# Optimization experiments

Measured on AMD Instinct MI355X. Metric: run time of the kernel, lower is better.

Reference implementation:

```python
import jax, jax.numpy as jnp
import numpy as np

B, S, D = 2, 2048, 1024
H = 16
DH = D // H  # 64


def setup_inputs() -> dict:
    key = jax.random.key(0)
    k1, k2, k3, k4, k5 = jax.random.split(key, 5)
    scale = 1.0 / np.sqrt(D)
    return {
        "x": jax.random.normal(k1, (B, S, D), dtype=jnp.float32),
        "w_in": jax.random.normal(k2, (3 * D, D), dtype=jnp.float32) * scale,
        "b_in": jax.random.normal(k3, (3 * D,), dtype=jnp.float32) * 0.02,
        "w_out": jax.random.normal(k4, (D, D), dtype=jnp.float32) * scale,
        "b_out": jax.random.normal(k5, (D,), dtype=jnp.float32) * 0.02,
        "mask": 1,
    }


def reference(x, w_in, b_in, w_out, b_out, mask):
    bs, seq_len, d_emb = x.shape
    # in_proj: torch Linear -> x @ W^T + b
    qkv = jnp.einsum("bsd,ed->bse", x, w_in) + b_in  # (B, S, 3D)
    q, k, v = jnp.split(qkv, 3, axis=-1)
    # (B, S, D) -> (B, H, S, DH)
    def heads(t):
        return t.reshape(bs, seq_len, H, DH).transpose(0, 2, 1, 3)
    q, k, v = heads(q), heads(k), heads(v)
    scores = jnp.einsum("bhqd,bhkd->bhqk", q, k)  # (B, H, S, S)
    if mask:
        causal = jnp.triu(jnp.ones((seq_len, seq_len), dtype=bool), k=1)
        scores = jnp.where(causal, -jnp.inf, scores)
    # original divides after masking; -inf / scale is still -inf
    scores = scores / jnp.sqrt(jnp.asarray(DH, dtype=scores.dtype))
    weights = jax.nn.softmax(scores, axis=-1)
    att = jnp.einsum("bhqk,bhkd->bhqd", weights, v)  # (B, H, S, DH)
    att = att.transpose(0, 2, 1, 3).reshape(bs, seq_len, d_emb)
    out = jnp.einsum("bsd,ed->bse", att, w_out) + b_out
    return out
```

## Files before the change

kernel.cpp:

```cpp
#include <hip/hip_runtime.h>
#include <hip/hip_bf16.h>
#include <stdint.h>


typedef __attribute__((ext_vector_type(8))) short bf16x8;
typedef __attribute__((ext_vector_type(4))) float f32x4;
typedef __attribute__((ext_vector_type(16))) float f32x16;
typedef __attribute__((ext_vector_type(4))) unsigned int u32x4;

typedef const __attribute__((address_space(1))) uint32_t* gp1_t;
typedef __attribute__((address_space(3))) uint32_t* lp3_t;

static __device__ __forceinline__ uint32_t cvtpk(float lo, float hi) {
  uint32_t r;
  asm("v_cvt_pk_bf16_f32 %0, %1, %2" : "=v"(r) : "v"(lo), "v"(hi));
  return r;
}
static __device__ __forceinline__ uint16_t f2b(float x) {
  return (uint16_t)cvtpk(x, x);
}
static __device__ __forceinline__ float fexp2(float x) {
  float r;
  asm("v_exp_f32 %0, %1" : "=v"(r) : "v"(x));
  return r;
}

template <int ISSUES>
static __device__ __forceinline__ void stage64(const uint16_t* __restrict__ g, int gstride,
                                               uint8_t* lds, int t) {
#pragma unroll
  for (int i = 0; i < ISSUES; ++i) {
    int p = i * 256 + t;
    int row = p >> 3, c = p & 7;
    const uint16_t* src = g + row * gstride + ((c ^ (row & 7)) << 3);
    __builtin_amdgcn_global_load_lds((gp1_t)src, (lp3_t)(lds + (p & ~63) * 16), 16, 0, 0);
  }
}

static __device__ __forceinline__ bf16x8 ld_frag(const uint8_t* lds, int row, int chunk) {
  return *(const bf16x8*)(lds + row * 128 + (((chunk) ^ (row & 7)) << 4));
}

__global__ __launch_bounds__(256) void cvt3(const float* __restrict__ a,
                                            const float* __restrict__ b,
                                            const float* __restrict__ c,
                                            uint16_t* __restrict__ oa,
                                            uint16_t* __restrict__ ob,
                                            uint16_t* __restrict__ oc) {
  int i = blockIdx.x * 256 + threadIdx.x;
  const float* src;
  uint16_t* dst;
  int j;
  if (i < 1048576)      { src = a; dst = oa; j = i; }
  else if (i < 1835008) { src = b; dst = ob; j = i - 1048576; }
  else                  { src = c; dst = oc; j = i - 1835008; }
  float4 v = ((const float4*)src)[j];
  uint2 o;
  o.x = cvtpk(v.x, v.y);
  o.y = cvtpk(v.z, v.w);
  ((uint2*)dst)[j] = o;
}

__global__ __launch_bounds__(256) void gemm_qkv(const uint16_t* __restrict__ A,
                                                const uint16_t* __restrict__ W,
                                                const float* __restrict__ bias,
                                                uint16_t* __restrict__ Qb,
                                                uint16_t* __restrict__ Kb,
                                                uint16_t* __restrict__ Vt) {
  __shared__ union {
    uint8_t stage[65536];
    uint16_t ot[128][136];
  } sm;
  int t = threadIdx.x, l = t & 63, w = t >> 6;
  int m0 = blockIdx.y * 128, n0 = blockIdx.x * 128;
  int wr = (w >> 1) * 64, wc = (w & 1) * 64;
  const f32x4 fz = {0.f, 0.f, 0.f, 0.f};
  f32x4 acc[4][4];
#pragma unroll
  for (int i = 0; i < 4; ++i)
#pragma unroll
    for (int j = 0; j < 4; ++j) acc[i][j] = fz;

  const uint16_t* Ab_ = A + m0 * 1024;
  const uint16_t* Wb_ = W + n0 * 1024;
  stage64<4>(Ab_, 1024, sm.stage, t);
  stage64<4>(Wb_, 1024, sm.stage + 16384, t);

  for (int kt = 0; kt < 16; ++kt) {
    int cur = kt & 1;
    uint8_t* curb = sm.stage + (cur << 15);
    asm volatile("s_waitcnt vmcnt(0)" ::: "memory");
    __syncthreads();
    if (kt + 1 < 16) {
      uint8_t* nb = sm.stage + ((cur ^ 1) << 15);
      stage64<4>(Ab_ + (kt + 1) * 64, 1024, nb, t);
      stage64<4>(Wb_ + (kt + 1) * 64, 1024, nb + 16384, t);
    }
#pragma unroll
    for (int ks = 0; ks < 2; ++ks) {
      bf16x8 a[4], b[4];
#pragma unroll
      for (int i = 0; i < 4; ++i) {
        a[i] = ld_frag(curb, wr + i * 16 + (l & 15), ks * 4 + (l >> 4));
        b[i] = ld_frag(curb + 16384, wc + i * 16 + (l & 15), ks * 4 + (l >> 4));
      }
#pragma unroll
      for (int i = 0; i < 4; ++i)
#pragma unroll
        for (int j = 0; j < 4; ++j)
          acc[i][j] = __builtin_amdgcn_mfma_f32_16x16x32_bf16(a[i], b[j], acc[i][j], 0, 0, 0);
    }
  }

  __syncthreads();
  const float CSQ = 0.18033688011112042f;
  int sec = n0 >> 10;
#pragma unroll
  for (int j = 0; j < 4; ++j) {
    int col = wc + j * 16 + (l & 15);
    float bv = bias[n0 + col];
#pragma unroll
    for (int i = 0; i < 4; ++i) {
      int rb = wr + i * 16 + ((l >> 4) << 2);
#pragma unroll
      for (int r = 0; r < 4; ++r) {
        int row = rb + r;
        float v = acc[i][j][r] + bv;
        if (sec == 0) v *= CSQ;
        if (sec == 2) {
          int rowp = (row & ~12) | ((row & 4) << 1) | ((row & 8) >> 1);
          sm.ot[col][rowp] = f2b(v);
        } else {
          sm.ot[row][col] = f2b(v);
        }
      }
    }
  }
  __syncthreads();

  int bb0 = m0 >> 11, sbase = m0 & 2047;
  int h0 = (n0 & 1023) >> 6;
  if (sec < 2) {
    uint16_t* dst0 = (sec == 0) ? Qb : Kb;
    int s_loc = t & 127, hh = t >> 7;
    const uint16_t* src = &sm.ot[s_loc][hh * 64];
    uint16_t* dst = dst0 + (((size_t)((bb0 * 16 + h0 + hh) * 2048 + sbase + s_loc)) << 6);
#pragma unroll
    for (int c = 0; c < 8; ++c)
      *(u32x4*)(dst + c * 8) = *(const u32x4*)(src + c * 8);
  } else {
    int re = t >> 1, scc = t & 1;
    int hh = re >> 6, dh = re & 63;
    const uint16_t* src = &sm.ot[re][scc * 64];
    uint16_t* dst = Vt + ((size_t)((bb0 * 16 + h0 + hh) * 64 + dh)) * 2048 + sbase + scc * 64;
#pragma unroll
    for (int c = 0; c < 8; ++c)
      *(u32x4*)(dst + c * 8) = *(const u32x4*)(src + c * 8);
  }
}

__global__ __launch_bounds__(256) void gemm_out(const uint16_t* __restrict__ A,
                                                const uint16_t* __restrict__ W,
                                                const float* __restrict__ bias,
                                                float* __restrict__ out) {
  __shared__ uint8_t sm[65536];
  int t = threadIdx.x, l = t & 63, w = t >> 6;
  int m0 = blockIdx.y * 128, n0 = blockIdx.x * 128;
  int wr = (w >> 1) * 64, wc = (w & 1) * 64;
  const f32x4 fz = {0.f, 0.f, 0.f, 0.f};
  f32x4 acc[4][4];
#pragma unroll
  for (int i = 0; i < 4; ++i)
#pragma unroll
    for (int j = 0; j < 4; ++j) acc[i][j] = fz;

  const uint16_t* Ab_ = A + m0 * 1024;
  const uint16_t* Wb_ = W + n0 * 1024;
  stage64<4>(Ab_, 1024, sm, t);
  stage64<4>(Wb_, 1024, sm + 16384, t);

  for (int kt = 0; kt < 16; ++kt) {
    int cur = kt & 1;
    uint8_t* curb = sm + (cur << 15);
    asm volatile("s_waitcnt vmcnt(0)" ::: "memory");
    __syncthreads();
    if (kt + 1 < 16) {
      uint8_t* nb = sm + ((cur ^ 1) << 15);
      stage64<4>(Ab_ + (kt + 1) * 64, 1024, nb, t);
      stage64<4>(Wb_ + (kt + 1) * 64, 1024, nb + 16384, t);
    }
#pragma unroll
    for (int ks = 0; ks < 2; ++ks) {
      bf16x8 a[4], b[4];
#pragma unroll
      for (int i = 0; i < 4; ++i) {
        a[i] = ld_frag(curb, wr + i * 16 + (l & 15), ks * 4 + (l >> 4));
        b[i] = ld_frag(curb + 16384, wc + i * 16 + (l & 15), ks * 4 + (l >> 4));
      }
#pragma unroll
      for (int i = 0; i < 4; ++i)
#pragma unroll
        for (int j = 0; j < 4; ++j)
          acc[i][j] = __builtin_amdgcn_mfma_f32_16x16x32_bf16(a[i], b[j], acc[i][j], 0, 0, 0);
    }
  }
#pragma unroll
  for (int j = 0; j < 4; ++j) {
    int e = n0 + wc + j * 16 + (l & 15);
    float bv = bias[e];
#pragma unroll
    for (int i = 0; i < 4; ++i) {
      int mb = m0 + wr + i * 16 + ((l >> 4) << 2);
#pragma unroll
      for (int r = 0; r < 4; ++r) {
        int m = mb + r;
        out[m * 1024 + e] = acc[i][j][r] + bv;
      }
    }
  }
}

__global__ __launch_bounds__(512) void attn(const uint16_t* __restrict__ Qb,
                                            const uint16_t* __restrict__ Kb,
                                            const uint16_t* __restrict__ Vt,
                                            uint16_t* __restrict__ Ab,
                                            const int* __restrict__ maskp) {
  __shared__ uint8_t smem[32768];
  int t = threadIdx.x, l = t & 63, w = t >> 6;
  int hi = l >> 5, ql = l & 31;
  int did = (int)blockIdx.x;
  int xcd = did & 7, idx = did >> 3;
  int bh = xcd * 4 + (idx >> 3);
  int p = idx & 7;
  int g = w >> 2, wg = w & 3;
  bool causal = (*maskp != 0);
  int st = g ? p : 15 - p;
  int ntg = causal ? 2 * (st + 1) : 32;
  int nth = causal ? 2 * (16 - p) : 32;
  int q0w = st * 128 + wg * 32;
  int q = q0w + ql;
  int bb = bh >> 4, h = bh & 15;

  const uint16_t* KpB = Kb + ((size_t)bh << 17);
  const uint16_t* VpB = Vt + ((size_t)bh << 17);

  bf16x8 qf[4];
  const uint16_t* Qp = Qb + (((size_t)bh * 2048 + q) << 6) + hi * 8;
#pragma unroll
  for (int ks = 0; ks < 4; ++ks) qf[ks] = *(const bf16x8*)(Qp + ks * 16);

  f32x16 acco[2];
#pragma unroll
  for (int r = 0; r < 16; ++r) { acco[0][r] = 0.f; acco[1][r] = 0.f; }
  float lsum = 0.f;

  stage64<1>(KpB, 64, smem, t);
  stage64<1>(VpB, 2048, smem + 8192, t);

  for (int tt = 0; tt < nth; ++tt) {
    int cur = tt & 1;
    asm volatile("s_waitcnt vmcnt(0)" ::: "memory");
    __syncthreads();
    if (tt + 1 < nth) {
      uint8_t* nb = smem + ((cur ^ 1) << 14);
      stage64<1>(KpB + ((size_t)(tt + 1) << 12), 64, nb, t);
      stage64<1>(VpB + (tt + 1) * 64, 2048, nb + 8192, t);
    }
    if (tt >= ntg || (causal && tt * 64 > q0w + 31)) continue;

    const uint8_t* Ks = smem + (cur << 14);
    const uint8_t* Vs = Ks + 8192;
    bf16x8 kf[2][4], vf[2][4];
#pragma unroll
    for (int ks = 0; ks < 4; ++ks) {
      kf[0][ks] = ld_frag(Ks, ql,      ks * 2 + hi);
      kf[1][ks] = ld_frag(Ks, 32 + ql, ks * 2 + hi);
      vf[0][ks] = ld_frag(Vs, ql,      ks * 2 + hi);
      vf[1][ks] = ld_frag(Vs, 32 + ql, ks * 2 + hi);
    }

    f32x16 sc[2];
#pragma unroll
    for (int r = 0; r < 16; ++r) { sc[0][r] = 0.f; sc[1][r] = 0.f; }
    __builtin_amdgcn_s_setprio(1);
#pragma unroll
    for (int ks = 0; ks < 4; ++ks)
      sc[0] = __builtin_amdgcn_mfma_f32_32x32x16_bf16(kf[0][ks], qf[ks], sc[0], 0, 0, 0);
#pragma unroll
    for (int ks = 0; ks < 4; ++ks)
      sc[1] = __builtin_amdgcn_mfma_f32_32x32x16_bf16(kf[1][ks], qf[ks], sc[1], 0, 0, 0);
    __builtin_amdgcn_s_setprio(0);

    bool nomask = (!causal) || (tt * 64 + 63 <= q0w);
    int qrel = q - tt * 64;
    float rs0 = 0.f, rs1 = 0.f, rs2 = 0.f, rs3 = 0.f;

#pragma unroll
    for (int r = 0; r < 16; ++r) {
      float v = sc[0][r];
      if (!nomask) {
        int kv = (r & 3) + 8 * (r >> 2) + 4 * hi;
        v = (kv <= qrel) ? v : -1e30f;
      }
      float e = fexp2(v);
      sc[0][r] = e;
      if (r & 1) rs1 += e; else rs0 += e;
    }

    __builtin_amdgcn_s_setprio(1);
#pragma unroll
    for (int ks = 0; ks < 2; ++ks) {
      int a8 = ks * 8;
      u32x4 wv = {cvtpk(sc[0][a8 + 0], sc[0][a8 + 1]),
                  cvtpk(sc[0][a8 + 2], sc[0][a8 + 3]),
                  cvtpk(sc[0][a8 + 4], sc[0][a8 + 5]),
                  cvtpk(sc[0][a8 + 6], sc[0][a8 + 7])};
      bf16x8 af = __builtin_bit_cast(bf16x8, wv);
      acco[0] = __builtin_amdgcn_mfma_f32_32x32x16_bf16(af, vf[0][ks], acco[0], 0, 0, 0);
      acco[1] = __builtin_amdgcn_mfma_f32_32x32x16_bf16(af, vf[1][ks], acco[1], 0, 0, 0);
    }
    __builtin_amdgcn_s_setprio(0);

#pragma unroll
    for (int r = 0; r < 16; ++r) {
      float v = sc[1][r];
      if (!nomask) {
        int kv = 32 + (r & 3) + 8 * (r >> 2) + 4 * hi;
        v = (kv <= qrel) ? v : -1e30f;
      }
      float e = fexp2(v);
      sc[1][r] = e;
      if (r & 1) rs3 += e; else rs2 += e;
    }

    __builtin_amdgcn_s_setprio(1);
#pragma unroll
    for (int ks = 0; ks < 2; ++ks) {
      int a8 = ks * 8;
      u32x4 wv = {cvtpk(sc[1][a8 + 0], sc[1][a8 + 1]),
                  cvtpk(sc[1][a8 + 2], sc[1][a8 + 3]),
                  cvtpk(sc[1][a8 + 4], sc[1][a8 + 5]),
                  cvtpk(sc[1][a8 + 6], sc[1][a8 + 7])};
      bf16x8 af = __builtin_bit_cast(bf16x8, wv);
      acco[0] = __builtin_amdgcn_mfma_f32_32x32x16_bf16(af, vf[0][ks + 2], acco[0], 0, 0, 0);
      acco[1] = __builtin_amdgcn_mfma_f32_32x32x16_bf16(af, vf[1][ks + 2], acco[1], 0, 0, 0);
    }
    __builtin_amdgcn_s_setprio(0);

    lsum += (rs0 + rs1) + (rs2 + rs3);
  }

  lsum += __shfl_xor(lsum, 32);
#pragma unroll
  for (int r = 0; r < 16; ++r) {
    int crow = (r & 3) + 8 * (r >> 2) + 4 * hi;
    float L = __shfl(lsum, crow);
    float inv = 1.0f / L;
    int qg = q0w + crow;
#pragma unroll
    for (int n = 0; n < 2; ++n)
      Ab[(((size_t)(bb * 2048 + qg)) << 10) + h * 64 + n * 32 + ql] = f2b(acco[n][r] * inv);
  }
}

extern "C" void kernel_launch(void* const* d_in, const int* in_sizes, int n_in,
                              void* d_out, int out_size, void* d_ws, size_t ws_size,
                              hipStream_t stream) {
  const float* x     = (const float*)d_in[0];
  const float* w_in  = (const float*)d_in[1];
  const float* b_in  = (const float*)d_in[2];
  const float* w_out = (const float*)d_in[3];
  const float* b_out = (const float*)d_in[4];
  const int*   mask  = (const int*)d_in[5];
  float* out = (float*)d_out;

  uint8_t* ws = (uint8_t*)d_ws;
  uint16_t* xb  = (uint16_t*)(ws);
  uint16_t* wib = (uint16_t*)(ws + (8u << 20));
  uint16_t* wob = (uint16_t*)(ws + (14u << 20));
  uint16_t* Qb  = (uint16_t*)(ws + (16u << 20));
  uint16_t* Kb  = (uint16_t*)(ws + (24u << 20));
  uint16_t* Vt  = (uint16_t*)(ws + (32u << 20));
  uint16_t* Ab  = (uint16_t*)(ws + (40u << 20));

  cvt3<<<8192, 256, 0, stream>>>(x, w_in, w_out, xb, wib, wob);
  gemm_qkv<<<dim3(24, 32), 256, 0, stream>>>(xb, wib, b_in, Qb, Kb, Vt);
  attn<<<256, 512, 0, stream>>>(Qb, Kb, Vt, Ab, mask);
  gemm_out<<<dim3(8, 32), 256, 0, stream>>>(Ab, wob, b_out, out);
}
```

Baseline: 124.8 us.

## Split attention KV range across two warp groups per query tile with LDS reduction

Before this change, each block paired two query tiles (st and 15-p) across its two 4-warp groups to balance causal work. Now each block owns one 128-row query tile, and the two warp groups split its KV range in half, each running its own double-buffered K/V staging. Partial output accumulators and row sums are merged through shared memory at the end. The grid doubles to 512 blocks to expose more parallelism, at the cost of doubled LDS per block (64KB), an extra reduction pass, and uneven block sizes across the causal triangle.

```diff
diff --git a/kernel.cpp b/kernel.cpp
--- a/kernel.cpp
+++ b/kernel.cpp
@@ -225,24 +225,25 @@
                                             const uint16_t* __restrict__ Vt,
                                             uint16_t* __restrict__ Ab,
                                             const int* __restrict__ maskp) {
-  __shared__ uint8_t smem[32768];
+  __shared__ uint8_t smem[65536];
   int t = threadIdx.x, l = t & 63, w = t >> 6;
   int hi = l >> 5, ql = l & 31;
+  int g = w >> 2, wg = w & 3;
+  int tl = t & 255;
   int did = (int)blockIdx.x;
   int xcd = did & 7, idx = did >> 3;
-  int bh = xcd * 4 + (idx >> 3);
-  int p = idx & 7;
-  int g = w >> 2, wg = w & 3;
+  int st = 15 - (idx >> 2);
+  int bh = xcd * 4 + (idx & 3);
   bool causal = (*maskp != 0);
-  int st = g ? p : 15 - p;
-  int ntg = causal ? 2 * (st + 1) : 32;
-  int nth = causal ? 2 * (16 - p) : 32;
+  int rounds = causal ? (st + 1) : 16;
+  int tile0 = g * rounds;
   int q0w = st * 128 + wg * 32;
   int q = q0w + ql;
   int bb = bh >> 4, h = bh & 15;
 
   const uint16_t* KpB = Kb + ((size_t)bh << 17);
   const uint16_t* VpB = Vt + ((size_t)bh << 17);
+  uint8_t* gbuf = smem + (g << 15);
 
   bf16x8 qf[4];
   const uint16_t* Qp = Qb + (((size_t)bh * 2048 + q) << 6) + hi * 8;
@@ -254,21 +255,22 @@
   for (int r = 0; r < 16; ++r) { acco[0][r] = 0.f; acco[1][r] = 0.f; }
   float lsum = 0.f;
 
-  stage64<1>(KpB, 64, smem, t);
-  stage64<1>(VpB, 2048, smem + 8192, t);
-
-  for (int tt = 0; tt < nth; ++tt) {
-    int cur = tt & 1;
+  stage64<2>(KpB + ((size_t)tile0 << 12), 64, gbuf, tl);
+  stage64<2>(VpB + tile0 * 64, 2048, gbuf + 8192, tl);
+
+  for (int rr = 0; rr < rounds; ++rr) {
+    int tt = tile0 + rr;
+    int cur = rr & 1;
     asm volatile("s_waitcnt vmcnt(0)" ::: "memory");
     __syncthreads();
-    if (tt + 1 < nth) {
-      uint8_t* nb = smem + ((cur ^ 1) << 14);
-      stage64<1>(KpB + ((size_t)(tt + 1) << 12), 64, nb, t);
-      stage64<1>(VpB + (tt + 1) * 64, 2048, nb + 8192, t);
-    }
-    if (tt >= ntg || (causal && tt * 64 > q0w + 31)) continue;
-
-    const uint8_t* Ks = smem + (cur << 14);
+    if (rr + 1 < rounds) {
+      uint8_t* nb = gbuf + ((cur ^ 1) << 14);
+      stage64<2>(KpB + ((size_t)(tt + 1) << 12), 64, nb, tl);
+      stage64<2>(VpB + (tt + 1) * 64, 2048, nb + 8192, tl);
+    }
+    if (causal && tt * 64 > q0w + 31) continue;
+
+    const uint8_t* Ks = gbuf + (cur << 14);
     const uint8_t* Vs = Ks + 8192;
     bf16x8 kf[2][4], vf[2][4];
 #pragma unroll
@@ -350,16 +352,36 @@
     lsum += (rs0 + rs1) + (rs2 + rs3);
   }
 
+  __syncthreads();
   lsum += __shfl_xor(lsum, 32);
-#pragma unroll
-  for (int r = 0; r < 16; ++r) {
-    int crow = (r & 3) + 8 * (r >> 2) + 4 * hi;
-    float L = __shfl(lsum, crow);
-    float inv = 1.0f / L;
-    int qg = q0w + crow;
-#pragma unroll
-    for (int n = 0; n < 2; ++n)
-      Ab[(((size_t)(bb * 2048 + qg)) << 10) + h * 64 + n * 32 + ql] = f2b(acco[n][r] * inv);
+  float (*oaccS)[64][33] = (float(*)[64][33])smem;
+  float (*lsumS)[64]     = (float(*)[64])(smem + 33792);
+  if (g == 1) {
+#pragma unroll
+    for (int r = 0; r < 16; ++r) {
+      oaccS[wg][l][r] = acco[0][r];
+      oaccS[wg][l][16 + r] = acco[1][r];
+    }
+    lsumS[wg][l] = lsum;
+  }
+  __syncthreads();
+  if (g == 0) {
+#pragma unroll
+    for (int r = 0; r < 16; ++r) {
+      acco[0][r] += oaccS[wg][l][r];
+      acco[1][r] += oaccS[wg][l][16 + r];
+    }
+    lsum += lsumS[wg][l];
+#pragma unroll
+    for (int r = 0; r < 16; ++r) {
+      int crow = (r & 3) + 8 * (r >> 2) + 4 * hi;
+      float L = __shfl(lsum, crow);
+      float inv = 1.0f / L;
+      int qg = q0w + crow;
+#pragma unroll
+      for (int n = 0; n < 2; ++n)
+        Ab[(((size_t)(bb * 2048 + qg)) << 10) + h * 64 + n * 32 + ql] = f2b(acco[n][r] * inv);
+    }
   }
 }
 
@@ -385,6 +407,6 @@
 
   cvt3<<<8192, 256, 0, stream>>>(x, w_in, w_out, xb, wib, wob);
   gemm_qkv<<<dim3(24, 32), 256, 0, stream>>>(xb, wib, b_in, Qb, Kb, Vt);
-  attn<<<256, 512, 0, stream>>>(Qb, Kb, Vt, Ab, mask);
+  attn<<<512, 512, 0, stream>>>(Qb, Kb, Vt, Ab, mask);
   gemm_out<<<dim3(8, 32), 256, 0, stream>>>(Ab, wob, b_out, out);
 }
```

Measured after the change: 115.7 us. 7.3% less time.
